# Kernel tuning notes

Hardware: AMD Instinct MI355X
Metric: run time of the kernel (lower is better)

Reference implementation:

```python
import jax, jax.numpy as jnp
import numpy as np

MOMENTUM = 0.8
EPSILON = 1e-05


def setup_inputs() -> dict:
    key = jax.random.key(0)
    k_x, = jax.random.split(key, 1)
    bs, C, H, W = 32, 3, 512, 512
    x = jax.random.normal(k_x, (bs, C, H, W), dtype=jnp.float32)
    gamma = jnp.ones((C,), dtype=jnp.float32)
    beta = jnp.zeros((C,), dtype=jnp.float32)
    running_mean = jnp.zeros((C,), dtype=jnp.float32)
    running_var = jnp.ones((C,), dtype=jnp.float32)
    return {"x": x, "gamma": gamma, "beta": beta,
            "running_mean": running_mean, "running_var": running_var}


def reference(x, gamma, beta, running_mean, running_var):
    # --- get_mean_var_fourier: batched ifft2 -> real -> per-channel stats ---
    # sx: [bs, C, H, W] real part of 2D inverse FFT per (batch, channel)
    sx = jnp.fft.ifft2(x, axes=(-2, -1)).real.astype(x.dtype)
    # per-channel mean/var over (batch, H, W) -- matches reshape(C,-1) stats
    mean = jnp.mean(sx, axis=(0, 2, 3))                      # [C]
    var = jnp.mean((sx - mean[None, :, None, None]) ** 2, axis=(0, 2, 3))  # [C]
    # --- running-stat update (training mode) ---
    rm = running_mean * MOMENTUM + (1.0 - MOMENTUM) * mean   # [C]
    rv = running_var * MOMENTUM + (1.0 - MOMENTUM) * var     # [C]
    # --- single-pass channel-wise affine normalize (fused) ---
    inv_std = 1.0 / jnp.sqrt(rv + EPSILON)                   # [C]
    out = (gamma * inv_std)[None, :, None, None] * (x - rm[None, :, None, None]) \
          + beta[None, :, None, None]
    return out
```

## Files before the change

kernel.cpp:

```cpp
#include <hip/hip_runtime.h>
#include <math.h>

#define BS 32
#define CH 3
#define HH 512
#define WW 512
#define HWSZ (HH * WW)
#define MOMENTUM 0.8
#define EPSILON 1e-5


constexpr int BPP = 16;
constexpr int ROWS_PER_BLK = 16;
constexpr int STAT_THREADS = 256;
constexpr int F4_PER_THREAD = ROWS_PER_BLK * (WW / 4) / STAT_THREADS;
constexpr int BATCH = 4;
constexpr int NBATCH = F4_PER_THREAD / BATCH;
constexpr int NBLOCKS = BS * CH * BPP;

__global__ __launch_bounds__(STAT_THREADS) void stats_kernel(
    const float* __restrict__ x, float4* __restrict__ partials) {
    const int plane = blockIdx.x / BPP;
    const int blk   = blockIdx.x % BPP;
    const float* __restrict__ base = x + (size_t)plane * HWSZ;
    const int tid = threadIdx.x;
    const int h0  = blk * ROWS_PER_BLK;

    float s1 = 0.f, s2 = 0.f, s3 = 0.f;

    for (int nb = 0; nb < NBATCH; ++nb) {
        float4 a[BATCH], p1[BATCH], p2[BATCH];
#pragma unroll
        for (int j = 0; j < BATCH; ++j) {
            const int idx  = tid + (nb * BATCH + j) * STAT_THREADS;
            const int r    = idx >> 7;
            const int col4 = idx & 127;
            const int o    = ((h0 + r) << 9) + (col4 << 2);
            const bool w0  = (col4 == 0);
            const int q1 = (HWSZ + 508 - o) & (HWSZ - 1);
            const int q2 = (HWSZ + (w0 ? 0 : 512) - o) & (HWSZ - 1);
            a[j]  = *reinterpret_cast<const float4*>(base + o);
            p1[j] = *reinterpret_cast<const float4*>(base + q1);
            p2[j] = *reinterpret_cast<const float4*>(base + q2);
        }
#pragma unroll
        for (int j = 0; j < BATCH; ++j) {
            const int idx = tid + (nb * BATCH + j) * STAT_THREADS;
            const int h   = h0 + (idx >> 7);
            const float4 a_ = a[j], p1_ = p1[j], p2_ = p2[j];
            const float asq = a_.x * a_.x + a_.y * a_.y + a_.z * a_.z + a_.w * a_.w;
            const float qsq = p1_.x * p1_.x + p1_.y * p1_.y + p1_.z * p1_.z + p1_.w * p1_.w;
            const float prd = a_.x * p2_.x + a_.y * p1_.w + a_.z * p1_.z + a_.w * p1_.y;
            const float two = (h == 0) ? 0.f : 1.f;
            s2 += asq + two * qsq;
            s3 += (h == 0 ? 1.f : 2.f) * prd;
            if (h == 0 && idx == 0) s1 += a_.x;
        }
    }

    if (blk == 0 && tid < 128) {
        const int o  = 256 * WW + tid * 4;
        const bool w0 = (tid == 0);
        const int q1 = (HWSZ + 508 - o) & (HWSZ - 1);
        const int q2 = (HWSZ + (w0 ? 0 : 512) - o) & (HWSZ - 1);
        const float4 a_  = *reinterpret_cast<const float4*>(base + o);
        const float4 p1_ = *reinterpret_cast<const float4*>(base + q1);
        const float4 p2_ = *reinterpret_cast<const float4*>(base + q2);
        s2 += a_.x * a_.x + a_.y * a_.y + a_.z * a_.z + a_.w * a_.w;
        s3 += a_.x * p2_.x + a_.y * p1_.w + a_.z * p1_.z + a_.w * p1_.y;
    }

#pragma unroll
    for (int off = 32; off > 0; off >>= 1) {
        s1 += __shfl_down(s1, off);
        s2 += __shfl_down(s2, off);
        s3 += __shfl_down(s3, off);
    }
    __shared__ float red[3][4];
    const int lane = tid & 63, wv = tid >> 6;
    if (lane == 0) { red[0][wv] = s1; red[1][wv] = s2; red[2][wv] = s3; }
    __syncthreads();
    if (tid == 0) {
        float4 p;
        p.x = red[0][0] + red[0][1] + red[0][2] + red[0][3];
        p.y = red[1][0] + red[1][1] + red[1][2] + red[1][3];
        p.z = red[2][0] + red[2][1] + red[2][2] + red[2][3];
        p.w = 0.f;
        partials[blockIdx.x] = p;
    }
}

__global__ __launch_bounds__(256) void finalize_kernel(
    const float4* __restrict__ partials,
    const float* __restrict__ gamma, const float* __restrict__ beta,
    const float* __restrict__ rmean, const float* __restrict__ rvar,
    float* __restrict__ ss) {
    const int c = blockIdx.x;
    const int tid = threadIdx.x;
    const int per_c = BS * BPP;
    double t1 = 0.0, t2 = 0.0, t3 = 0.0;
    for (int k = tid; k < per_c; k += 256) {
        const int b = k / BPP, blk = k % BPP;
        const float4 p = partials[(b * CH + c) * BPP + blk];
        t1 += (double)p.x; t2 += (double)p.y; t3 += (double)p.z;
    }
#pragma unroll
    for (int off = 32; off > 0; off >>= 1) {
        t1 += __shfl_down(t1, off);
        t2 += __shfl_down(t2, off);
        t3 += __shfl_down(t3, off);
    }
    __shared__ double red[3][4];
    const int lane = tid & 63, wv = tid >> 6;
    if (lane == 0) { red[0][wv] = t1; red[1][wv] = t2; red[2][wv] = t3; }
    __syncthreads();
    if (tid == 0) {
        const double S1 = red[0][0] + red[0][1] + red[0][2] + red[0][3];
        const double S2 = red[1][0] + red[1][1] + red[1][2] + red[1][3];
        const double S3 = red[2][0] + red[2][1] + red[2][2] + red[2][3];
        const double N = (double)BS * (double)HWSZ;
        const double mean = S1 / N;
        const double ex2  = (S2 + S3) / (2.0 * N * (double)HWSZ);
        const double var  = ex2 - mean * mean;
        const double rm = (double)rmean[c] * MOMENTUM + (1.0 - MOMENTUM) * mean;
        const double rv = (double)rvar[c]  * MOMENTUM + (1.0 - MOMENTUM) * var;
        const double inv_std = 1.0 / sqrt(rv + EPSILON);
        const float scale = (float)((double)gamma[c] * inv_std);
        const float shift = (float)((double)beta[c] - (double)scale * rm);
        ss[c * 2 + 0] = scale;
        ss[c * 2 + 1] = shift;
    }
}

__global__ __launch_bounds__(256) void norm_kernel(
    const float* __restrict__ x, const float* __restrict__ ss,
    float* __restrict__ out) {
    float sc[CH], sh[CH];
#pragma unroll
    for (int c = 0; c < CH; ++c) { sc[c] = ss[c * 2]; sh[c] = ss[c * 2 + 1]; }
    const int n4 = BS * CH * HWSZ / 4;
    const int stride = gridDim.x * blockDim.x;
    for (int i4 = blockIdx.x * blockDim.x + threadIdx.x; i4 < n4; i4 += stride) {
        const int c = (i4 >> 16) % CH;
        const float4 v = reinterpret_cast<const float4*>(x)[i4];
        const float s = sc[c], t = sh[c];
        float4 o;
        o.x = fmaf(v.x, s, t);
        o.y = fmaf(v.y, s, t);
        o.z = fmaf(v.z, s, t);
        o.w = fmaf(v.w, s, t);
        reinterpret_cast<float4*>(out)[i4] = o;
    }
}

extern "C" void kernel_launch(void* const* d_in, const int* in_sizes, int n_in,
                              void* d_out, int out_size, void* d_ws, size_t ws_size,
                              hipStream_t stream) {
    const float* x     = (const float*)d_in[0];
    const float* gamma = (const float*)d_in[1];
    const float* beta  = (const float*)d_in[2];
    const float* rmean = (const float*)d_in[3];
    const float* rvar  = (const float*)d_in[4];
    float* out = (float*)d_out;

    float4* partials = (float4*)d_ws;
    float*  ss = (float*)((char*)d_ws + NBLOCKS * 16);

    stats_kernel<<<NBLOCKS, STAT_THREADS, 0, stream>>>(x, partials);
    finalize_kernel<<<CH, 256, 0, stream>>>(partials, gamma, beta, rmean, rvar, ss);
    norm_kernel<<<2048, 256, 0, stream>>>(x, ss, out);
}
```

Baseline: 59.92 us.

## Fuse stats, finalize and normalize into one cooperative kernel holding x in registers

```diff
diff --git a/kernel.cpp b/kernel.cpp
--- a/kernel.cpp
+++ b/kernel.cpp
@@ -1,5 +1,8 @@
 #include <hip/hip_runtime.h>
+#include <hip/hip_cooperative_groups.h>
 #include <math.h>
+
+namespace cg = cooperative_groups;
 
 #define BS 32
 #define CH 3
@@ -10,6 +13,187 @@
 #define EPSILON 1e-5
 
 
+constexpr int TPB   = 512;
+constexpr int NBLK  = 256;
+constexpr int NTHR  = NBLK * TPB;
+constexpr int JN    = 24;
+constexpr int R256  = BS * CH * (WW / 4);
+
+__global__ __launch_bounds__(TPB, 2) void fused_kernel(
+    const float* __restrict__ x, const float* __restrict__ gamma,
+    const float* __restrict__ beta, const float* __restrict__ rmean,
+    const float* __restrict__ rvar, float* __restrict__ out,
+    float* __restrict__ ws) {
+    const int tid = threadIdx.x;
+    const int g   = blockIdx.x * TPB + tid;
+    const int p0  = g >> 15;
+    const int mf  = g & 32767;
+    const int h   = mf >> 7;
+    const bool w0 = (mf & 127) == 0;
+    const int o   = mf * 4;
+    const int q1  = (HWSZ + 508 - o) & (HWSZ - 1);
+    const int q2  = (HWSZ + (w0 ? 0 : 512) - o) & (HWSZ - 1);
+    const float f3 = (h == 0) ? 1.f : 2.f;
+    const float fpp = (h == 0) ? 0.f : 1.f;
+
+    float4 a[JN], p[JN];
+    float sb1[3] = {0.f, 0.f, 0.f};
+    float sb2[3] = {0.f, 0.f, 0.f};
+    float sb3[3] = {0.f, 0.f, 0.f};
+
+#pragma unroll
+    for (int j = 0; j < JN; ++j) {
+        const float* bp = x + (size_t)(p0 + 4 * j) * HWSZ;
+        a[j] = *reinterpret_cast<const float4*>(bp + o);
+        p[j] = *reinterpret_cast<const float4*>(bp + q1);
+        const float4 c = *reinterpret_cast<const float4*>(bp + q2);
+        const float4 A = a[j], P = p[j];
+        const float asq = A.x * A.x + A.y * A.y + A.z * A.z + A.w * A.w;
+        const float psq = P.x * P.x + P.y * P.y + P.z * P.z + P.w * P.w;
+        const float prd = A.x * c.x + A.y * P.w + A.z * P.z + A.w * P.y;
+        sb2[j % 3] += asq + fpp * psq;
+        sb3[j % 3] += f3 * prd;
+        if (mf == 0) sb1[j % 3] += A.x;
+    }
+
+    const bool ex = (g < R256);
+    float4 a6 = make_float4(0.f, 0.f, 0.f, 0.f);
+    int ch6 = 0;
+    size_t o6g = 0;
+    if (ex) {
+        const int pl = g >> 7;
+        const int cf = g & 127;
+        const int oo = 131072 + 4 * cf;
+        const bool w06 = (cf == 0);
+        const int qq1 = (HWSZ + 508 - oo) & (HWSZ - 1);
+        const int qq2 = (HWSZ + (w06 ? 0 : 512) - oo) & (HWSZ - 1);
+        const float* bp = x + (size_t)pl * HWSZ;
+        a6 = *reinterpret_cast<const float4*>(bp + oo);
+        const float4 P = *reinterpret_cast<const float4*>(bp + qq1);
+        const float4 c = *reinterpret_cast<const float4*>(bp + qq2);
+        const float asq = a6.x * a6.x + a6.y * a6.y + a6.z * a6.z + a6.w * a6.w;
+        const float prd = a6.x * c.x + a6.y * P.w + a6.z * P.z + a6.w * P.y;
+        ch6 = pl % 3;
+        const int b6 = (ch6 - (p0 % 3) + 3) % 3;
+        if (b6 == 0)      { sb2[0] += asq; sb3[0] += prd; }
+        else if (b6 == 1) { sb2[1] += asq; sb3[1] += prd; }
+        else              { sb2[2] += asq; sb3[2] += prd; }
+        o6g = (size_t)pl * HWSZ + oo;
+    }
+
+    float v[9];
+    {
+        const int r = p0 % 3;
+        if (r == 0) {
+            v[0]=sb1[0]; v[1]=sb2[0]; v[2]=sb3[0];
+            v[3]=sb1[1]; v[4]=sb2[1]; v[5]=sb3[1];
+            v[6]=sb1[2]; v[7]=sb2[2]; v[8]=sb3[2];
+        } else if (r == 1) {
+            v[0]=sb1[2]; v[1]=sb2[2]; v[2]=sb3[2];
+            v[3]=sb1[0]; v[4]=sb2[0]; v[5]=sb3[0];
+            v[6]=sb1[1]; v[7]=sb2[1]; v[8]=sb3[1];
+        } else {
+            v[0]=sb1[1]; v[1]=sb2[1]; v[2]=sb3[1];
+            v[3]=sb1[2]; v[4]=sb2[2]; v[5]=sb3[2];
+            v[6]=sb1[0]; v[7]=sb2[0]; v[8]=sb3[0];
+        }
+    }
+
+    __shared__ float red[8][9];
+    __shared__ float ssh[6];
+#pragma unroll
+    for (int off = 32; off > 0; off >>= 1)
+#pragma unroll
+        for (int i = 0; i < 9; ++i) v[i] += __shfl_down(v[i], off);
+    const int wv = tid >> 6, ln = tid & 63;
+    if (ln == 0)
+#pragma unroll
+        for (int i = 0; i < 9; ++i) red[wv][i] = v[i];
+    __syncthreads();
+    if (tid == 0) {
+        float t[9];
+#pragma unroll
+        for (int i = 0; i < 9; ++i)
+            t[i] = red[0][i] + red[1][i] + red[2][i] + red[3][i]
+                 + red[4][i] + red[5][i] + red[6][i] + red[7][i];
+        float* bws = ws + (size_t)blockIdx.x * 12;
+        *reinterpret_cast<float4*>(bws)     = make_float4(t[0], t[1], t[2], t[3]);
+        *reinterpret_cast<float4*>(bws + 4) = make_float4(t[4], t[5], t[6], t[7]);
+        *reinterpret_cast<float4*>(bws + 8) = make_float4(t[8], 0.f, 0.f, 0.f);
+    }
+    __threadfence();
+    cg::this_grid().sync();
+
+    float u[9] = {0.f,0.f,0.f,0.f,0.f,0.f,0.f,0.f,0.f};
+    if (tid < NBLK) {
+        const float* bws = ws + (size_t)tid * 12;
+        const float4 A = *reinterpret_cast<const float4*>(bws);
+        const float4 B = *reinterpret_cast<const float4*>(bws + 4);
+        const float4 C = *reinterpret_cast<const float4*>(bws + 8);
+        u[0]=A.x; u[1]=A.y; u[2]=A.z; u[3]=A.w;
+        u[4]=B.x; u[5]=B.y; u[6]=B.z; u[7]=B.w; u[8]=C.x;
+    }
+#pragma unroll
+    for (int off = 32; off > 0; off >>= 1)
+#pragma unroll
+        for (int i = 0; i < 9; ++i) u[i] += __shfl_down(u[i], off);
+    if (ln == 0)
+#pragma unroll
+        for (int i = 0; i < 9; ++i) red[wv][i] = u[i];
+    __syncthreads();
+    if (tid == 0) {
+#pragma unroll
+        for (int c = 0; c < CH; ++c) {
+            const double S1 = (double)(red[0][3*c+0] + red[1][3*c+0] + red[2][3*c+0] + red[3][3*c+0]);
+            const double S2 = (double)(red[0][3*c+1] + red[1][3*c+1] + red[2][3*c+1] + red[3][3*c+1]);
+            const double S3 = (double)(red[0][3*c+2] + red[1][3*c+2] + red[2][3*c+2] + red[3][3*c+2]);
+            const double N = (double)BS * (double)HWSZ;
+            const double mean = S1 / N;
+            const double ex2  = (S2 + S3) / (2.0 * N * (double)HWSZ);
+            const double var  = ex2 - mean * mean;
+            const double rm = (double)rmean[c] * MOMENTUM + (1.0 - MOMENTUM) * mean;
+            const double rv = (double)rvar[c]  * MOMENTUM + (1.0 - MOMENTUM) * var;
+            const double inv_std = 1.0 / sqrt(rv + EPSILON);
+            const float scale = (float)((double)gamma[c] * inv_std);
+            const float shift = (float)((double)beta[c] - (double)scale * rm);
+            ssh[2*c]   = scale;
+            ssh[2*c+1] = shift;
+        }
+    }
+    __syncthreads();
+
+    float sc[3], sh[3];
+#pragma unroll
+    for (int b = 0; b < 3; ++b) {
+        const int ch = (p0 + b) % 3;
+        sc[b] = ssh[2*ch]; sh[b] = ssh[2*ch+1];
+    }
+#pragma unroll
+    for (int j = 0; j < JN; ++j) {
+        float* bo = out + (size_t)(p0 + 4 * j) * HWSZ;
+        const float s = sc[j % 3], t = sh[j % 3];
+        const float4 A = a[j];
+        float4 oa;
+        oa.x = fmaf(A.x, s, t); oa.y = fmaf(A.y, s, t);
+        oa.z = fmaf(A.z, s, t); oa.w = fmaf(A.w, s, t);
+        *reinterpret_cast<float4*>(bo + o) = oa;
+        if (h != 0) {
+            const float4 P = p[j];
+            float4 op;
+            op.x = fmaf(P.x, s, t); op.y = fmaf(P.y, s, t);
+            op.z = fmaf(P.z, s, t); op.w = fmaf(P.w, s, t);
+            *reinterpret_cast<float4*>(bo + q1) = op;
+        }
+    }
+    if (ex) {
+        const float s = ssh[2*ch6], t = ssh[2*ch6+1];
+        float4 oa;
+        oa.x = fmaf(a6.x, s, t); oa.y = fmaf(a6.y, s, t);
+        oa.z = fmaf(a6.z, s, t); oa.w = fmaf(a6.w, s, t);
+        *reinterpret_cast<float4*>(out + o6g) = oa;
+    }
+}
+
 constexpr int BPP = 16;
 constexpr int ROWS_PER_BLK = 16;
 constexpr int STAT_THREADS = 256;
@@ -25,9 +209,7 @@
     const float* __restrict__ base = x + (size_t)plane * HWSZ;
     const int tid = threadIdx.x;
     const int h0  = blk * ROWS_PER_BLK;
-
     float s1 = 0.f, s2 = 0.f, s3 = 0.f;
-
     for (int nb = 0; nb < NBATCH; ++nb) {
         float4 a[BATCH], p1[BATCH], p2[BATCH];
 #pragma unroll
@@ -48,16 +230,15 @@
             const int idx = tid + (nb * BATCH + j) * STAT_THREADS;
             const int h   = h0 + (idx >> 7);
             const float4 a_ = a[j], p1_ = p1[j], p2_ = p2[j];
-            const float asq = a_.x * a_.x + a_.y * a_.y + a_.z * a_.z + a_.w * a_.w;
-            const float qsq = p1_.x * p1_.x + p1_.y * p1_.y + p1_.z * p1_.z + p1_.w * p1_.w;
-            const float prd = a_.x * p2_.x + a_.y * p1_.w + a_.z * p1_.z + a_.w * p1_.y;
+            const float asq = a_.x*a_.x + a_.y*a_.y + a_.z*a_.z + a_.w*a_.w;
+            const float qsq = p1_.x*p1_.x + p1_.y*p1_.y + p1_.z*p1_.z + p1_.w*p1_.w;
+            const float prd = a_.x*p2_.x + a_.y*p1_.w + a_.z*p1_.z + a_.w*p1_.y;
             const float two = (h == 0) ? 0.f : 1.f;
             s2 += asq + two * qsq;
             s3 += (h == 0 ? 1.f : 2.f) * prd;
             if (h == 0 && idx == 0) s1 += a_.x;
         }
     }
-
     if (blk == 0 && tid < 128) {
         const int o  = 256 * WW + tid * 4;
         const bool w0 = (tid == 0);
@@ -66,10 +247,9 @@
         const float4 a_  = *reinterpret_cast<const float4*>(base + o);
         const float4 p1_ = *reinterpret_cast<const float4*>(base + q1);
         const float4 p2_ = *reinterpret_cast<const float4*>(base + q2);
-        s2 += a_.x * a_.x + a_.y * a_.y + a_.z * a_.z + a_.w * a_.w;
-        s3 += a_.x * p2_.x + a_.y * p1_.w + a_.z * p1_.z + a_.w * p1_.y;
-    }
-
+        s2 += a_.x*a_.x + a_.y*a_.y + a_.z*a_.z + a_.w*a_.w;
+        s3 += a_.x*p2_.x + a_.y*p1_.w + a_.z*p1_.z + a_.w*p1_.y;
+    }
 #pragma unroll
     for (int off = 32; off > 0; off >>= 1) {
         s1 += __shfl_down(s1, off);
@@ -145,10 +325,8 @@
         const float4 v = reinterpret_cast<const float4*>(x)[i4];
         const float s = sc[c], t = sh[c];
         float4 o;
-        o.x = fmaf(v.x, s, t);
-        o.y = fmaf(v.y, s, t);
-        o.z = fmaf(v.z, s, t);
-        o.w = fmaf(v.w, s, t);
+        o.x = fmaf(v.x, s, t); o.y = fmaf(v.y, s, t);
+        o.z = fmaf(v.z, s, t); o.w = fmaf(v.w, s, t);
         reinterpret_cast<float4*>(out)[i4] = o;
     }
 }
@@ -162,10 +340,16 @@
     const float* rmean = (const float*)d_in[3];
     const float* rvar  = (const float*)d_in[4];
     float* out = (float*)d_out;
+    float* ws  = (float*)d_ws;
+
+    void* args[] = {(void*)&x, (void*)&gamma, (void*)&beta, (void*)&rmean,
+                    (void*)&rvar, (void*)&out, (void*)&ws};
+    const hipError_t e = hipLaunchCooperativeKernel(
+        (const void*)fused_kernel, dim3(NBLK), dim3(TPB), args, 0, stream);
+    if (e == hipSuccess) return;
 
     float4* partials = (float4*)d_ws;
     float*  ss = (float*)((char*)d_ws + NBLOCKS * 16);
-
     stats_kernel<<<NBLOCKS, STAT_THREADS, 0, stream>>>(x, partials);
     finalize_kernel<<<CH, 256, 0, stream>>>(partials, gamma, beta, rmean, rvar, ss);
     norm_kernel<<<2048, 256, 0, stream>>>(x, ss, out);
```

Result: slower. 112.9 us (+88.4%).
